# Performance work log

Measured on AMD Instinct MI355X. Metric: run time of the kernel, lower is better.

Reference implementation:

```python
import jax, jax.numpy as jnp
import numpy as np

N_HEADS = 32
ROPE_THETA = 10000.0


def _rope_cos_sin(sl, head_dim, dtype):
    # inv_freq over even dims, HF/Llama convention: emb = concat(freqs, freqs)
    inv_freq = 1.0 / (ROPE_THETA ** (jnp.arange(0, head_dim, 2, dtype=jnp.float32) / head_dim))
    pos = jnp.arange(sl, dtype=jnp.float32)
    freqs = pos[:, None] * inv_freq[None, :]            # [sl, hd/2]
    emb = jnp.concatenate([freqs, freqs], axis=-1)       # [sl, hd]
    return jnp.cos(emb).astype(dtype), jnp.sin(emb).astype(dtype)


def _rotate_half(x):
    h = x.shape[-1] // 2
    return jnp.concatenate([-x[..., h:], x[..., :h]], axis=-1)


def setup_inputs() -> dict:
    key = jax.random.key(0)
    ks = jax.random.split(key, 5)
    bs, sl, hs = 2, 2048, 4096
    scale = hs ** -0.5
    return {
        "hidden_states": jax.random.normal(ks[0], (bs, sl, hs), jnp.float32),
        "wq": jax.random.normal(ks[1], (hs, hs), jnp.float32) * scale,
        "wk": jax.random.normal(ks[2], (hs, hs), jnp.float32) * scale,
        "wv": jax.random.normal(ks[3], (hs, hs), jnp.float32) * scale,
        "wo": jax.random.normal(ks[4], (hs, hs), jnp.float32) * scale,
    }


def reference(hidden_states, wq, wk, wv, wo):
    bs, sl, hs = hidden_states.shape
    hd = hs // N_HEADS
    # QKV projections (nn.Linear without bias: x @ W.T; here W stored as [in,out])
    q = hidden_states @ wq
    k = hidden_states @ wk
    v = hidden_states @ wv
    # [bs, sl, H, hd]
    q = q.reshape(bs, sl, N_HEADS, hd)
    k = k.reshape(bs, sl, N_HEADS, hd)
    v = v.reshape(bs, sl, N_HEADS, hd)
    # Vectorized RoPE across the whole sequence (original loops per position)
    cos, sin = _rope_cos_sin(sl, hd, hidden_states.dtype)   # [sl, hd]
    cos = cos[None, :, None, :]
    sin = sin[None, :, None, :]
    q = q * cos + _rotate_half(q) * sin
    k = k * cos + _rotate_half(k) * sin
    # causal SDPA, [bs, H, sl, hd]
    q = q.transpose(0, 2, 1, 3)
    k = k.transpose(0, 2, 1, 3)
    v = v.transpose(0, 2, 1, 3)
    scores = jnp.einsum("bhqd,bhkd->bhqk", q, k) / jnp.sqrt(jnp.asarray(hd, q.dtype))
    causal = jnp.tril(jnp.ones((sl, sl), dtype=bool))
    scores = jnp.where(causal[None, None], scores, jnp.finfo(scores.dtype).min)
    attn = jax.nn.softmax(scores, axis=-1)
    out = jnp.einsum("bhqk,bhkd->bhqd", attn, v)
    out = out.transpose(0, 2, 1, 3).reshape(bs, sl, hs)
    return out @ wo
```

## Files before the change

kernel.cpp:

```cpp
#include <hip/hip_runtime.h>
#include <cstdint>
#include <cstddef>

#define SL 2048
#define BS 2
#define NH 32
#define HD 128
#define HS 4096
#define NTOK 4096
#define LDQ 12288

typedef __attribute__((ext_vector_type(8))) short short8;
typedef __attribute__((ext_vector_type(4))) float f32x4;
typedef __attribute__((ext_vector_type(4))) unsigned short u16x4;
typedef __attribute__((ext_vector_type(8))) unsigned short u16x8;

static __device__ __forceinline__ unsigned short f2bf(float f) {
    unsigned int u = __builtin_bit_cast(unsigned int, f);
    u = u + 0x7FFFu + ((u >> 16) & 1u);
    return (unsigned short)(u >> 16);
}
static __device__ __forceinline__ float bf2f(unsigned short h) {
    unsigned int u = ((unsigned int)h) << 16;
    return __builtin_bit_cast(float, u);
}

static __device__ __forceinline__ f32x4 mfma16(short8 a, short8 b, f32x4 c) {
    return __builtin_amdgcn_mfma_f32_16x16x32_bf16(a, b, c, 0, 0, 0);
}

static __device__ __forceinline__ void gload_lds16(const void* g, void* dst) {
    __builtin_amdgcn_global_load_lds(
        (const __attribute__((address_space(1))) unsigned int*)g,
        (__attribute__((address_space(3))) unsigned int*)dst,
        16, 0, 0);
}

__global__ void k_convert(const float* __restrict__ in, unsigned short* __restrict__ out, int n8) {
    int stride = gridDim.x * blockDim.x;
    for (int i = blockIdx.x * blockDim.x + threadIdx.x; i < n8; i += stride) {
        const f32x4* p = (const f32x4*)in + (size_t)i * 2;
        f32x4 a = p[0], b = p[1];
        u16x8 o;
        o[0] = f2bf(a[0]); o[1] = f2bf(a[1]); o[2] = f2bf(a[2]); o[3] = f2bf(a[3]);
        o[4] = f2bf(b[0]); o[5] = f2bf(b[1]); o[6] = f2bf(b[2]); o[7] = f2bf(b[3]);
        *((u16x8*)out + i) = o;
    }
}

__global__ void k_transpose_w4(const float* __restrict__ w0, const float* __restrict__ w1,
                               const float* __restrict__ w2, const float* __restrict__ w3,
                               unsigned short* __restrict__ wtbase) {
    __shared__ float t[32][33];
    int z = blockIdx.z;
    const float* w = (z == 0) ? w0 : (z == 1) ? w1 : (z == 2) ? w2 : w3;
    unsigned short* wt = wtbase + (size_t)z * HS * HS;
    int r0 = blockIdx.y << 5, c0 = blockIdx.x << 5;
    int tr = threadIdx.x >> 3;
    int tc = (threadIdx.x & 7) << 2;
    f32x4 v = *(const f32x4*)(w + (size_t)(r0 + tr) * HS + c0 + tc);
    t[tr][tc + 0] = v[0]; t[tr][tc + 1] = v[1]; t[tr][tc + 2] = v[2]; t[tr][tc + 3] = v[3];
    __syncthreads();
    u16x4 o;
    o[0] = f2bf(t[tc + 0][tr]); o[1] = f2bf(t[tc + 1][tr]);
    o[2] = f2bf(t[tc + 2][tr]); o[3] = f2bf(t[tc + 3][tr]);
    *(u16x4*)(wt + (size_t)(c0 + tr) * HS + r0 + tc) = o;
}

#define REG(b, w) ((b) * 65536 + (w) * 16384)

template <typename OutT>
__global__ __launch_bounds__(512, 2) void k_gemm256(
    const unsigned short* __restrict__ A,
    const unsigned short* __restrict__ Bt,
    OutT* __restrict__ C,
    int M, int N, int K)
{
    __shared__ char lds[131072];
    char* ldsb = lds;
    int tiles_n = N >> 8;
    int bid = blockIdx.x;
    int q8 = gridDim.x >> 3;
    bid = (bid & 7) * q8 + (bid >> 3);
    int tm = bid / tiles_n, tn = bid % tiles_n;
    int tid = threadIdx.x, lane = tid & 63, wave = tid >> 6;
    int l15 = lane & 15, kh = lane >> 4;
    int wm = wave >> 2, wn = wave & 3;
    int row0 = tm << 8, col0 = tn << 8;
    f32x4 acc[8][4] = {};

    int sr = tid >> 3;
    int scb = (tid & 7) << 4;
    int scol = (scb ^ ((sr & 7) << 4)) >> 1;
    const unsigned short* Abase0 = A + (size_t)(row0 + sr) * K + scol;
    const unsigned short* Bbase0 = Bt + (size_t)(col0 + sr) * K + scol;

    int rswz = (l15 & 7) << 4;
    int afb = wm * 16384 + l15 * 128 + ((kh * 16) ^ rswz);
    int bfb = 32768 + ((wn >> 1) * 16384) + (((wn & 1) * 64 + l15) * 128) + ((kh * 16) ^ rswz);

    short8 af[4][2], bfr[4][2];

#define STAGE(R, Gp) do { \
    gload_lds16((Gp),                ldsb + (R) + tid * 16); \
    gload_lds16((Gp) + (size_t)64 * K, ldsb + (R) + 8192 + tid * 16); } while (0)

#define READ_A(buf, g) { _Pragma("unroll") for (int mq = 0; mq < 4; ++mq) \
    _Pragma("unroll") for (int ks = 0; ks < 2; ++ks) \
        af[mq][ks] = *(const short8*)(ldsb + (buf) * 65536 + ((afb + (g) * 8192 + mq * 2048) ^ (ks * 64))); }

#define READ_B(buf) { _Pragma("unroll") for (int n = 0; n < 4; ++n) \
    _Pragma("unroll") for (int ks = 0; ks < 2; ++ks) \
        bfr[n][ks] = *(const short8*)(ldsb + (buf) * 65536 + ((bfb + n * 2048) ^ (ks * 64))); }

#define MFMA_Q(g, nh) { _Pragma("unroll") for (int mq = 0; mq < 4; ++mq) \
    _Pragma("unroll") for (int n2 = 0; n2 < 2; ++n2) { \
        acc[(g)*4+mq][(nh)*2+n2] = mfma16(af[mq][0], bfr[(nh)*2+n2][0], acc[(g)*4+mq][(nh)*2+n2]); \
        acc[(g)*4+mq][(nh)*2+n2] = mfma16(af[mq][1], bfr[(nh)*2+n2][1], acc[(g)*4+mq][(nh)*2+n2]); } }

#define LGKM0() do { asm volatile("s_waitcnt lgkmcnt(0)" ::: "memory"); \
                     __builtin_amdgcn_sched_barrier(0); } while (0)
#define BAR() __builtin_amdgcn_s_barrier()

    STAGE(REG(0, 2), Bbase0);
    STAGE(REG(0, 3), Bbase0 + (size_t)128 * K);
    STAGE(REG(0, 0), Abase0);
    STAGE(REG(0, 1), Abase0 + (size_t)128 * K);
    STAGE(REG(1, 2), Bbase0 + 64);
    STAGE(REG(1, 3), Bbase0 + (size_t)128 * K + 64);
    STAGE(REG(1, 0), Abase0 + 64);
    asm volatile("s_waitcnt vmcnt(6)" ::: "memory");
    BAR();

    int nkt = K >> 6;
    int niter = nkt >> 1;
    #pragma unroll 1
    for (int t = 0; t < niter; ++t) {
        int kt1 = 2 * t + 1, kt2 = 2 * t + 2, kt3 = 2 * t + 3;
        bool s2 = kt2 < nkt, s3 = kt3 < nkt;
        READ_B(0); READ_A(0, 0);
        STAGE(REG(1, 1), Abase0 + (size_t)128 * K + (size_t)kt1 * 64);
        BAR(); LGKM0();
        __builtin_amdgcn_s_setprio(1); MFMA_Q(0, 0); __builtin_amdgcn_s_setprio(0);
        BAR();
        if (s2) STAGE(REG(0, 2), Bbase0 + (size_t)kt2 * 64);
        BAR();
        __builtin_amdgcn_s_setprio(1); MFMA_Q(0, 1); __builtin_amdgcn_s_setprio(0);
        BAR();
        READ_A(0, 1);
        if (s2) STAGE(REG(0, 3), Bbase0 + (size_t)128 * K + (size_t)kt2 * 64);
        BAR(); LGKM0();
        __builtin_amdgcn_s_setprio(1); MFMA_Q(1, 0); __builtin_amdgcn_s_setprio(0);
        BAR();
        if (s2) STAGE(REG(0, 0), Abase0 + (size_t)kt2 * 64);
        BAR();
        __builtin_amdgcn_s_setprio(1); MFMA_Q(1, 1); __builtin_amdgcn_s_setprio(0);
        if (s2) { asm volatile("s_waitcnt vmcnt(6)" ::: "memory"); }
        else    { asm volatile("s_waitcnt vmcnt(0)" ::: "memory"); }
        BAR();
        READ_B(1); READ_A(1, 0);
        if (s2) STAGE(REG(0, 1), Abase0 + (size_t)128 * K + (size_t)kt2 * 64);
        BAR(); LGKM0();
        __builtin_amdgcn_s_setprio(1); MFMA_Q(0, 0); __builtin_amdgcn_s_setprio(0);
        BAR();
        if (s3) STAGE(REG(1, 2), Bbase0 + (size_t)kt3 * 64);
        BAR();
        __builtin_amdgcn_s_setprio(1); MFMA_Q(0, 1); __builtin_amdgcn_s_setprio(0);
        BAR();
        READ_A(1, 1);
        if (s3) STAGE(REG(1, 3), Bbase0 + (size_t)128 * K + (size_t)kt3 * 64);
        BAR(); LGKM0();
        __builtin_amdgcn_s_setprio(1); MFMA_Q(1, 0); __builtin_amdgcn_s_setprio(0);
        BAR();
        if (s3) STAGE(REG(1, 0), Abase0 + (size_t)kt3 * 64);
        BAR();
        __builtin_amdgcn_s_setprio(1); MFMA_Q(1, 1); __builtin_amdgcn_s_setprio(0);
        if (s3) { asm volatile("s_waitcnt vmcnt(6)" ::: "memory"); }
        else    { asm volatile("s_waitcnt vmcnt(0)" ::: "memory"); }
        BAR();
    }

    #pragma unroll
    for (int m = 0; m < 8; ++m)
        #pragma unroll
        for (int n = 0; n < 4; ++n)
            #pragma unroll
            for (int rr = 0; rr < 4; ++rr) {
                int row = row0 + wm * 128 + m * 16 + kh * 4 + rr;
                int col = col0 + wn * 64 + n * 16 + l15;
                float v = acc[m][n][rr];
                if constexpr (sizeof(OutT) == 2) C[(size_t)row * N + col] = (OutT)f2bf(v);
                else                             C[(size_t)row * N + col] = v;
            }
#undef STAGE
#undef READ_A
#undef READ_B
#undef MFMA_Q
#undef LGKM0
#undef BAR
}

__global__ void k_rope(unsigned short* __restrict__ QKV) {
    const float SCALE = 0.08838834764831845f;
    int i = blockIdx.x * blockDim.x + threadIdx.x;
    int q4 = i & 15;
    int head = (i >> 4) & (NH - 1);
    int tok = i >> 9;
    int s = tok & (SL - 1);
    int d0 = q4 << 2;
    size_t base = (size_t)tok * LDQ + head * HD;
    unsigned short* Q = QKV + base;
    unsigned short* K = QKV + base + HS;
    float cs[4], sn[4];
    #pragma unroll
    for (int j = 0; j < 4; j++) {
        float invf = expf(-(float)(d0 + j) * 0.14391156831212787f);
        float ang = (float)s * invf;
        sn[j] = sinf(ang); cs[j] = cosf(ang);
    }
    {
        u16x4 lo = *(u16x4*)(Q + d0);
        u16x4 hi = *(u16x4*)(Q + d0 + 64);
        u16x4 nlo, nhi;
        #pragma unroll
        for (int j = 0; j < 4; j++) {
            float x0 = bf2f(lo[j]), x1 = bf2f(hi[j]);
            nlo[j] = f2bf((x0 * cs[j] - x1 * sn[j]) * SCALE);
            nhi[j] = f2bf((x1 * cs[j] + x0 * sn[j]) * SCALE);
        }
        *(u16x4*)(Q + d0) = nlo;
        *(u16x4*)(Q + d0 + 64) = nhi;
    }
    {
        u16x4 lo = *(u16x4*)(K + d0);
        u16x4 hi = *(u16x4*)(K + d0 + 64);
        u16x4 nlo, nhi;
        #pragma unroll
        for (int j = 0; j < 4; j++) {
            float x0 = bf2f(lo[j]), x1 = bf2f(hi[j]);
            nlo[j] = f2bf(x0 * cs[j] - x1 * sn[j]);
            nhi[j] = f2bf(x1 * cs[j] + x0 * sn[j]);
        }
        *(u16x4*)(K + d0) = nlo;
        *(u16x4*)(K + d0 + 64) = nhi;
    }
}

__global__ void k_transpose_v(const unsigned short* __restrict__ QKV, unsigned short* __restrict__ Vt) {
    __shared__ unsigned short t[32][36];
    int bh = blockIdx.z; int b = bh >> 5, h = bh & 31;
    int s0 = blockIdx.x << 5, d0 = blockIdx.y << 5;
    int tr = threadIdx.x >> 3, tc = (threadIdx.x & 7) << 2;
    u16x4 v = *(const u16x4*)(QKV + (size_t)(b * SL + s0 + tr) * LDQ + 2 * HS + h * HD + d0 + tc);
    t[tr][tc + 0] = v[0]; t[tr][tc + 1] = v[1]; t[tr][tc + 2] = v[2]; t[tr][tc + 3] = v[3];
    __syncthreads();
    u16x4 o;
    o[0] = t[tc + 0][tr]; o[1] = t[tc + 1][tr]; o[2] = t[tc + 2][tr]; o[3] = t[tc + 3][tr];
    *(u16x4*)(Vt + ((size_t)(b * NH + h) * HD + d0 + tr) * SL + s0 + tc) = o;
}

__global__ __launch_bounds__(256, 4) void k_attn(
    const unsigned short* __restrict__ QKV,
    const unsigned short* __restrict__ Vt,
    unsigned short* __restrict__ O)
{
    __shared__ unsigned short Ks[64 * 128];
    __shared__ unsigned short Vs[2][128 * 64];
    __shared__ unsigned short Ps[4][16][36];
    int qt = (int)(gridDim.x - 1) - (int)blockIdx.x;
    int bh = blockIdx.y;
    int b = bh >> 5, h = bh & 31;
    int tid = threadIdx.x, lane = tid & 63, wave = tid >> 6;
    int l15 = lane & 15, kh = lane >> 4;
    int qrow0 = (qt << 6) + (wave << 4);
    short8 qf[4];
    {
        const unsigned short* qp = QKV + ((size_t)(b * SL) + qrow0 + l15) * LDQ + h * HD + kh * 8;
        #pragma unroll
        for (int f = 0; f < 4; ++f) qf[f] = *(const short8*)(qp + f * 32);
    }
    f32x4 oacc[8] = {};
    float m[4] = {-1e30f, -1e30f, -1e30f, -1e30f};
    float lsum[4] = {0.f, 0.f, 0.f, 0.f};
    int ksrow = tid >> 4, kchunk = tid & 15;
    int vsrow = tid >> 3, vchunk = tid & 7;
    const unsigned short* Kbase = QKV + HS + (size_t)(b * SL) * LDQ + h * HD;
    const unsigned short* Vbase = Vt + (size_t)(b * NH + h) * HD * (size_t)SL;
    char* KsW = (char*)Ks + (wave << 10);

    #pragma unroll
    for (int c = 0; c < 4; ++c) {
        int kr = c * 16 + ksrow;
        gload_lds16(Kbase + (size_t)kr * LDQ + ((kchunk ^ (kr & 7)) << 3), KsW + c * 4096);
        int vr = c * 32 + vsrow;
        gload_lds16(Vbase + (size_t)vr * SL + ((vchunk ^ (vr & 7)) << 3),
                    (char*)Vs[0] + (wave << 10) + c * 4096);
    }
    int buf = 0;
    for (int kt = 0; kt <= qt; ++kt) {
        __syncthreads();
        f32x4 sfr[4];
        __builtin_amdgcn_s_setprio(1);
        #pragma unroll
        for (int c = 0; c < 4; ++c) {
            f32x4 acc = {};
            int krow = c * 16 + l15;
            #pragma unroll
            for (int f = 0; f < 4; ++f) {
                short8 kf = *(const short8*)((const char*)Ks + krow * 256 + ((((f << 2) + kh) ^ (krow & 7)) << 4));
                acc = mfma16(qf[f], kf, acc);
            }
            sfr[c] = acc;
        }
        __builtin_amdgcn_s_setprio(0);
        __syncthreads();
        if (kt < qt) {
            #pragma unroll
            for (int c = 0; c < 4; ++c) {
                int kr = c * 16 + ksrow;
                gload_lds16(Kbase + (size_t)(((kt + 1) << 6) + kr) * LDQ + ((kchunk ^ (kr & 7)) << 3),
                            KsW + c * 4096);
                int vr = c * 32 + vsrow;
                gload_lds16(Vbase + (size_t)vr * SL + ((kt + 1) << 6) + ((vchunk ^ (vr & 7)) << 3),
                            (char*)Vs[buf ^ 1] + (wave << 10) + c * 4096);
            }
        }
        float pm[4] = {-1e30f, -1e30f, -1e30f, -1e30f};
        if (kt == qt) {
            #pragma unroll
            for (int c = 0; c < 4; ++c) {
                int kkg = (kt << 6) + c * 16 + l15;
                #pragma unroll
                for (int r = 0; r < 4; ++r) {
                    int qg = qrow0 + kh * 4 + r;
                    float v = sfr[c][r];
                    v = (kkg > qg) ? -1e30f : v;
                    sfr[c][r] = v;
                    pm[r] = fmaxf(pm[r], v);
                }
            }
        } else {
            #pragma unroll
            for (int c = 0; c < 4; ++c)
                #pragma unroll
                for (int r = 0; r < 4; ++r) pm[r] = fmaxf(pm[r], sfr[c][r]);
        }
        #pragma unroll
        for (int off = 1; off < 16; off <<= 1)
            #pragma unroll
            for (int r = 0; r < 4; ++r) pm[r] = fmaxf(pm[r], __shfl_xor(pm[r], off, 64));
        bool ok = true;
        #pragma unroll
        for (int r = 0; r < 4; ++r) ok = ok && (pm[r] <= m[r] + 8.0f);
        if (!__all(ok)) {
            #pragma unroll
            for (int r = 0; r < 4; ++r) {
                float mn = fmaxf(m[r], pm[r]);
                float alpha = __expf(m[r] - mn);
                m[r] = mn;
                lsum[r] *= alpha;
                #pragma unroll
                for (int db = 0; db < 8; ++db) oacc[db][r] *= alpha;
            }
        }
        float rs[4] = {0.f, 0.f, 0.f, 0.f};
        #pragma unroll
        for (int c = 0; c < 4; ++c)
            #pragma unroll
            for (int r = 0; r < 4; ++r) {
                float p = __expf(sfr[c][r] - m[r]);
                sfr[c][r] = p;
                rs[r] += p;
            }
        #pragma unroll
        for (int off = 1; off < 16; off <<= 1)
            #pragma unroll
            for (int r = 0; r < 4; ++r) rs[r] += __shfl_xor(rs[r], off, 64);
        #pragma unroll
        for (int r = 0; r < 4; ++r) lsum[r] += rs[r];
        short8 pa[2];
        #pragma unroll
        for (int half = 0; half < 2; ++half) {
            #pragma unroll
            for (int c = 0; c < 2; ++c)
                #pragma unroll
                for (int r = 0; r < 4; ++r)
                    Ps[wave][kh * 4 + r][c * 16 + l15] = f2bf(sfr[half * 2 + c][r]);
            pa[half] = *(const short8*)(&Ps[wave][l15][kh * 8]);
        }
        const char* vb = (const char*)Vs[buf];
        __builtin_amdgcn_s_setprio(1);
        #pragma unroll
        for (int db = 0; db < 8; ++db) {
            int vrow = db * 16 + l15;
            #pragma unroll
            for (int f = 0; f < 2; ++f) {
                short8 vf = *(const short8*)(vb + vrow * 128 + ((((f << 2) + kh) ^ (vrow & 7)) << 4));
                oacc[db] = mfma16(pa[f], vf, oacc[db]);
            }
        }
        __builtin_amdgcn_s_setprio(0);
        buf ^= 1;
    }
    #pragma unroll
    for (int db = 0; db < 8; ++db)
        #pragma unroll
        for (int r = 0; r < 4; ++r) {
            int qg = qrow0 + kh * 4 + r;
            float v = oacc[db][r] / lsum[r];
            O[((size_t)(b * SL) + qg) * HS + h * HD + db * 16 + l15] = f2bf(v);
        }
}

extern "C" void kernel_launch(void* const* d_in, const int* in_sizes, int n_in,
                              void* d_out, int out_size, void* d_ws, size_t ws_size,
                              hipStream_t stream)
{
    const float* X  = (const float*)d_in[0];
    const float* Wq = (const float*)d_in[1];
    const float* Wk = (const float*)d_in[2];
    const float* Wv = (const float*)d_in[3];
    const float* Wo = (const float*)d_in[4];
    float* out = (float*)d_out;
    const size_t SLAB = (size_t)NTOK * HS * 2;
    char* ws = (char*)d_ws;
    unsigned short* Xb  = (unsigned short*)(ws + 0 * SLAB);
    unsigned short* Wqt = (unsigned short*)(ws + 1 * SLAB);
    unsigned short* Wot = (unsigned short*)(ws + 4 * SLAB);
    unsigned short* QKV = (unsigned short*)(ws + 5 * SLAB);
    unsigned short* Vtb = Xb;
    unsigned short* Ob  = Wqt;

    k_convert<<<2048, 256, 0, stream>>>(X, Xb, NTOK * HS / 8);
    k_transpose_w4<<<dim3(128, 128, 4), 256, 0, stream>>>(Wq, Wk, Wv, Wo, Wqt);
    k_gemm256<unsigned short><<<768, 512, 0, stream>>>(Xb, Wqt, QKV, NTOK, 3 * HS, HS);
    k_rope<<<NTOK * NH * 16 / 256, 256, 0, stream>>>(QKV);
    k_transpose_v<<<dim3(SL / 32, HD / 32, BS * NH), 256, 0, stream>>>(QKV, Vtb);
    k_attn<<<dim3(SL / 64, BS * NH), 256, 0, stream>>>(QKV, Vtb, Ob);
    k_gemm256<float><<<256, 512, 0, stream>>>(Ob, Wot, out, NTOK, HS, HS);
}
```

Measured before the change: 876.0 us.

## Split B-fragment LDS reads across phases and fold log2e into Q scale for exp2

The GEMM main loop now reads B fragments in two halves and stages A tiles at different points, with a partial lgkmcnt wait and a shallower vmcnt depth. This redistributes LDS reads and global loads across MFMA phases to improve overlap. Separately, the attention softmax folds log2(e) into the Q scale applied in RoPE and switches to a native exp2 intrinsic, adjusting the rescale threshold to match. This removes a multiply per exponential, but the reduced prefetch depth may expose more global memory latency.

```diff
diff --git a/kernel.cpp b/kernel.cpp
--- a/kernel.cpp
+++ b/kernel.cpp
@@ -23,6 +23,9 @@
 static __device__ __forceinline__ float bf2f(unsigned short h) {
     unsigned int u = ((unsigned int)h) << 16;
     return __builtin_bit_cast(float, u);
+}
+static __device__ __forceinline__ float fexp2(float x) {
+    return __builtin_amdgcn_exp2f(x);
 }
 
 static __device__ __forceinline__ f32x4 mfma16(short8 a, short8 b, f32x4 c) {
@@ -109,7 +112,7 @@
     _Pragma("unroll") for (int ks = 0; ks < 2; ++ks) \
         af[mq][ks] = *(const short8*)(ldsb + (buf) * 65536 + ((afb + (g) * 8192 + mq * 2048) ^ (ks * 64))); }
 
-#define READ_B(buf) { _Pragma("unroll") for (int n = 0; n < 4; ++n) \
+#define READ_B2(buf, p) { _Pragma("unroll") for (int n = 2*(p); n < 2*(p)+2; ++n) \
     _Pragma("unroll") for (int ks = 0; ks < 2; ++ks) \
         bfr[n][ks] = *(const short8*)(ldsb + (buf) * 65536 + ((bfb + n * 2048) ^ (ks * 64))); }
 
@@ -120,7 +123,10 @@
 
 #define LGKM0() do { asm volatile("s_waitcnt lgkmcnt(0)" ::: "memory"); \
                      __builtin_amdgcn_sched_barrier(0); } while (0)
+#define LGKM8() asm volatile("s_waitcnt lgkmcnt(8)" ::: "memory")
 #define BAR() __builtin_amdgcn_s_barrier()
+#define PRIO1() __builtin_amdgcn_s_setprio(1)
+#define PRIO0() __builtin_amdgcn_s_setprio(0)
 
     STAGE(REG(0, 2), Bbase0);
     STAGE(REG(0, 3), Bbase0 + (size_t)128 * K);
@@ -128,8 +134,7 @@
     STAGE(REG(0, 1), Abase0 + (size_t)128 * K);
     STAGE(REG(1, 2), Bbase0 + 64);
     STAGE(REG(1, 3), Bbase0 + (size_t)128 * K + 64);
-    STAGE(REG(1, 0), Abase0 + 64);
-    asm volatile("s_waitcnt vmcnt(6)" ::: "memory");
+    asm volatile("s_waitcnt vmcnt(4)" ::: "memory");
     BAR();
 
     int nkt = K >> 6;
@@ -138,44 +143,48 @@
     for (int t = 0; t < niter; ++t) {
         int kt1 = 2 * t + 1, kt2 = 2 * t + 2, kt3 = 2 * t + 3;
         bool s2 = kt2 < nkt, s3 = kt3 < nkt;
-        READ_B(0); READ_A(0, 0);
+        READ_B2(0, 0); READ_A(0, 0);
+        STAGE(REG(1, 0), Abase0 + (size_t)kt1 * 64);
+        LGKM8();
+        BAR(); LGKM0();
+        PRIO1(); MFMA_Q(0, 0); PRIO0();
+        BAR();
+        READ_B2(0, 1);
         STAGE(REG(1, 1), Abase0 + (size_t)128 * K + (size_t)kt1 * 64);
         BAR(); LGKM0();
-        __builtin_amdgcn_s_setprio(1); MFMA_Q(0, 0); __builtin_amdgcn_s_setprio(0);
-        BAR();
+        PRIO1(); MFMA_Q(0, 1); PRIO0();
+        BAR();
+        READ_A(0, 1);
         if (s2) STAGE(REG(0, 2), Bbase0 + (size_t)kt2 * 64);
-        BAR();
-        __builtin_amdgcn_s_setprio(1); MFMA_Q(0, 1); __builtin_amdgcn_s_setprio(0);
-        BAR();
-        READ_A(0, 1);
+        BAR(); LGKM0();
+        PRIO1(); MFMA_Q(1, 0); PRIO0();
+        BAR();
         if (s2) STAGE(REG(0, 3), Bbase0 + (size_t)128 * K + (size_t)kt2 * 64);
-        BAR(); LGKM0();
-        __builtin_amdgcn_s_setprio(1); MFMA_Q(1, 0); __builtin_amdgcn_s_setprio(0);
-        BAR();
+        BAR();
+        PRIO1(); MFMA_Q(1, 1); PRIO0();
+        if (s2) { asm volatile("s_waitcnt vmcnt(4)" ::: "memory"); }
+        else    { asm volatile("s_waitcnt vmcnt(0)" ::: "memory"); }
+        BAR();
+        READ_B2(1, 0); READ_A(1, 0);
         if (s2) STAGE(REG(0, 0), Abase0 + (size_t)kt2 * 64);
-        BAR();
-        __builtin_amdgcn_s_setprio(1); MFMA_Q(1, 1); __builtin_amdgcn_s_setprio(0);
-        if (s2) { asm volatile("s_waitcnt vmcnt(6)" ::: "memory"); }
-        else    { asm volatile("s_waitcnt vmcnt(0)" ::: "memory"); }
-        BAR();
-        READ_B(1); READ_A(1, 0);
+        LGKM8();
+        BAR(); LGKM0();
+        PRIO1(); MFMA_Q(0, 0); PRIO0();
+        BAR();
+        READ_B2(1, 1);
         if (s2) STAGE(REG(0, 1), Abase0 + (size_t)128 * K + (size_t)kt2 * 64);
         BAR(); LGKM0();
-        __builtin_amdgcn_s_setprio(1); MFMA_Q(0, 0); __builtin_amdgcn_s_setprio(0);
-        BAR();
+        PRIO1(); MFMA_Q(0, 1); PRIO0();
+        BAR();
+        READ_A(1, 1);
         if (s3) STAGE(REG(1, 2), Bbase0 + (size_t)kt3 * 64);
-        BAR();
-        __builtin_amdgcn_s_setprio(1); MFMA_Q(0, 1); __builtin_amdgcn_s_setprio(0);
-        BAR();
-        READ_A(1, 1);
+        BAR(); LGKM0();
+        PRIO1(); MFMA_Q(1, 0); PRIO0();
+        BAR();
         if (s3) STAGE(REG(1, 3), Bbase0 + (size_t)128 * K + (size_t)kt3 * 64);
-        BAR(); LGKM0();
-        __builtin_amdgcn_s_setprio(1); MFMA_Q(1, 0); __builtin_amdgcn_s_setprio(0);
-        BAR();
-        if (s3) STAGE(REG(1, 0), Abase0 + (size_t)kt3 * 64);
-        BAR();
-        __builtin_amdgcn_s_setprio(1); MFMA_Q(1, 1); __builtin_amdgcn_s_setprio(0);
-        if (s3) { asm volatile("s_waitcnt vmcnt(6)" ::: "memory"); }
+        BAR();
+        PRIO1(); MFMA_Q(1, 1); PRIO0();
+        if (s3) { asm volatile("s_waitcnt vmcnt(4)" ::: "memory"); }
         else    { asm volatile("s_waitcnt vmcnt(0)" ::: "memory"); }
         BAR();
     }
@@ -194,14 +203,17 @@
             }
 #undef STAGE
 #undef READ_A
-#undef READ_B
+#undef READ_B2
 #undef MFMA_Q
 #undef LGKM0
+#undef LGKM8
 #undef BAR
+#undef PRIO1
+#undef PRIO0
 }
 
 __global__ void k_rope(unsigned short* __restrict__ QKV) {
-    const float SCALE = 0.08838834764831845f;
+    const float SCALE = 0.12751779544166854f;
     int i = blockIdx.x * blockDim.x + threadIdx.x;
     int q4 = i & 15;
     int head = (i >> 4) & (NH - 1);
@@ -351,12 +363,12 @@
             for (int r = 0; r < 4; ++r) pm[r] = fmaxf(pm[r], __shfl_xor(pm[r], off, 64));
         bool ok = true;
         #pragma unroll
-        for (int r = 0; r < 4; ++r) ok = ok && (pm[r] <= m[r] + 8.0f);
+        for (int r = 0; r < 4; ++r) ok = ok && (pm[r] <= m[r] + 11.5f);
         if (!__all(ok)) {
             #pragma unroll
             for (int r = 0; r < 4; ++r) {
                 float mn = fmaxf(m[r], pm[r]);
-                float alpha = __expf(m[r] - mn);
+                float alpha = fexp2(m[r] - mn);
                 m[r] = mn;
                 lsum[r] *= alpha;
                 #pragma unroll
@@ -368,7 +380,7 @@
         for (int c = 0; c < 4; ++c)
             #pragma unroll
             for (int r = 0; r < 4; ++r) {
-                float p = __expf(sfr[c][r] - m[r]);
+                float p = fexp2(sfr[c][r] - m[r]);
                 sfr[c][r] = p;
                 rs[r] += p;
             }
```

After: 870.9 us. About the same (-0.6%).
